# Performance work log

Measured on AMD Instinct MI355X. Metric: run time of the kernel, lower is better.

## Reference

```python
import jax, jax.numpy as jnp
import numpy as np
import math

B, W, N = 48, 100, 1000
EMB, H, QKV, LOCAL = 128, 8, 16, 100
L = LOCAL + 1  # depot + local_size neighbors


def pos_enc(length):
    # sinusoidal positional encoding, emb_dim even so no pad needed
    nts = EMB // 2
    inv = jnp.exp(jnp.arange(nts, dtype=jnp.float32) * (-math.log(10000.0) / max(nts - 1, 1)))
    pos = jnp.arange(length, dtype=jnp.float32)
    st = pos[:, None] * inv[None, :]
    return jnp.concatenate([jnp.sin(st), jnp.cos(st)], axis=1)  # [length, EMB]


def setup_inputs() -> dict:
    key = jax.random.key(0)
    ks = jax.random.split(key, 11)
    return {
        "theta": jax.random.uniform(ks[0], (B, W, N), dtype=jnp.float32),
        "dist": jax.random.uniform(ks[1], (B, W, N), dtype=jnp.float32),
        "xy": jax.random.uniform(ks[2], (B, W, N, 2), dtype=jnp.float32),
        "norm_demand": jax.random.uniform(ks[3], (B, W, N), dtype=jnp.float32),
        "ninf_mask": jnp.zeros((B, W, N), jnp.float32),
        "init_w": jax.random.normal(ks[4], (3, EMB), dtype=jnp.float32) * 0.1,
        "init_b": jnp.zeros((EMB,), jnp.float32),
        "cur_token": jax.random.uniform(ks[5], (EMB,), minval=-1.0, maxval=1.0, dtype=jnp.float32),
        "Wq": jax.random.normal(ks[6], (EMB, H * QKV), dtype=jnp.float32) * 0.05,
        "Wk": jax.random.normal(ks[7], (EMB, H * QKV), dtype=jnp.float32) * 0.05,
        "Wv": jax.random.normal(ks[8], (EMB, H * QKV), dtype=jnp.float32) * 0.05,
        "Wc_w": jax.random.normal(ks[9], (H * QKV, EMB), dtype=jnp.float32) * 0.05,
        "Wc_b": jnp.zeros((EMB,), jnp.float32),
    }


def reference(theta, dist, xy, norm_demand, ninf_mask, init_w, init_b, cur_token, Wq, Wk, Wv, Wc_w, Wc_b):
    # depot always masked: dist -= mask => depot distance -> +inf
    mask = ninf_mask.at[:, :, 0].set(-jnp.inf)
    dist_eff = dist - mask  # [B,W,N]

    # k smallest distances among non-depot nodes (topk largest=False)
    neg_vals, idx0 = jax.lax.top_k(-dist_eff[:, :, 1:], LOCAL)
    dvals = -neg_vals
    dvals = jnp.where(jnp.isinf(dvals), 0.0, dvals)
    norm_on = (jnp.max(dvals, axis=-1) != 0.0)[..., None]          # [B,W,1]
    norm_fac = jnp.max(dvals, axis=-1, keepdims=True) + 1e-6       # [B,W,1]

    depot = jnp.zeros((B, W, 1), idx0.dtype)
    idx = jnp.concatenate([depot, idx0 + 1], axis=-1)              # [B,W,L]

    g = lambda a: jnp.take_along_axis(a, idx, axis=-1)
    sd = g(dist_eff)
    sdem = g(norm_demand)
    sm = g(ninf_mask)
    sx = g(xy[..., 0])
    sy = g(xy[..., 1])

    # zero out inf entries (the masked depot slot)
    infm = jnp.isinf(sd)
    sdem = jnp.where(infm, 0.0, sdem)
    sx = jnp.where(infm, 0.0, sx)
    sy = jnp.where(infm, 0.0, sy)

    # per-(b,w) coordinate normalization by max local distance
    sx = jnp.where(norm_on, sx / norm_fac, sx)
    sy = jnp.where(norm_on, sy / norm_fac, sy)

    # euclidean + demand => 3 input features
    sorted_input = jnp.stack([sx, sy, sdem], axis=-1)              # [B,W,L,3]
    init_k = sorted_input @ init_w + init_b + pos_enc(L)[None, None]  # [B,W,L,EMB]

    # cur_token is identical for every (b,w) -> shared query per head
    q = (cur_token @ Wq).reshape(H, QKV)
    k = (init_k @ Wk).reshape(B, W, L, H, QKV)
    v = (init_k @ Wv).reshape(B, W, L, H, QKV)

    score = jnp.einsum('hd,bwlhd->bwhl', q, k) / float(np.sqrt(QKV)) + sm[:, :, None, :]
    attn = jax.nn.softmax(score, axis=-1)
    out = jnp.einsum('bwhl,bwlhd->bwhd', attn, v).reshape(B, W, H * QKV)

    mh = out @ Wc_w + Wc_b                                         # [B,W,EMB]
    score2 = jnp.einsum('bwe,bwle->bwl', mh, init_k) / float(np.sqrt(EMB))

    bi = jnp.arange(B)[:, None, None]
    wi = jnp.arange(W)[None, :, None]
    return jnp.zeros((B, W, N), score2.dtype).at[bi, wi, idx].set(score2)
```

## Files before the change

### kernel.cpp

```cpp
#include <hip/hip_runtime.h>
#include <math.h>

#define Bb   48
#define Ww   100
#define Nn   1000
#define EMB  128
#define Hh   8
#define LL   101
#define LOCALK 100
#define TPB  128
#define PPB  2

typedef float f4v __attribute__((ext_vector_type(4)));

#define WS_A    0
#define WS_PE   1024
#define WS_AC   13952
#define WS_WVI  13984
#define WS_PEA  14496
#define WS_PVT  15304
#define WS_PET  28232

#define AR_SIZE 7840
#define AR_SEL  5088
#define AR_PERM 5492
#define AR_SMK  5592
#define AR_F3   5996
#define AR_MHF  7208
#define AR_COEF 7720
#define AR_CM   7816

#define WSYNC() do { __builtin_amdgcn_wave_barrier(); asm volatile("" ::: "memory"); } while (0)

__device__ __forceinline__ unsigned f2key(float x) {
    unsigned u = __float_as_uint(x);
    return (u & 0x80000000u) ? ~u : (u | 0x80000000u);
}
__device__ __forceinline__ float key2f(unsigned k) {
    unsigned u = (k & 0x80000000u) ? (k & 0x7fffffffu) : ~k;
    return __uint_as_float(u);
}

__global__ void setup1(const float* __restrict__ cur, const float* __restrict__ Wq,
                       const float* __restrict__ Wk, const float* __restrict__ iw,
                       const float* __restrict__ ib, const float* __restrict__ Wv,
                       float* __restrict__ ws) {
    const int t = threadIdx.x, b = blockIdx.x;
    if (b == 0) {
        __shared__ float qs[EMB];
        __shared__ float as_[Hh * EMB];
        if (t < EMB) {
            float acc = 0.f;
            for (int e = 0; e < EMB; ++e) acc += cur[e] * Wq[e * EMB + t];
            qs[t] = acc;
        }
        __syncthreads();
        for (int i = t; i < Hh * EMB; i += 256) {
            int h = i >> 7, e = i & 127;
            float acc = 0.f;
            for (int d = 0; d < 16; ++d) acc += Wk[e * EMB + h * 16 + d] * qs[h * 16 + d];
            acc *= 0.25f;
            as_[i] = acc; ws[WS_A + i] = acc;
        }
        __syncthreads();
        if (t < 32) {
            int i = t >> 3, h = t & 7;
            const float* src = (i == 0) ? iw : (i == 1) ? iw + EMB : (i == 2) ? iw + 2 * EMB : ib;
            float acc = 0.f;
            for (int e = 0; e < EMB; ++e) acc += src[e] * as_[h * EMB + e];
            ws[WS_AC + t] = acc;
        }
    } else {
        int base = (b - 1) * 256 + t;
        const float kneg = -0.14619587891040738f;
        if (base < LL * EMB) {
            int l = base >> 7, c = base & 127, ic = c & 63;
            float inv = expf((float)ic * kneg);
            float v = (float)l * inv;
            ws[WS_PE + base] = (c < 64) ? sinf(v) : cosf(v);
        } else if (base < LL * EMB + 512) {
            int j = base - LL * EMB;
            int iv = j >> 7, hd = j & 127;
            const float* src = (iv == 0) ? iw : (iv == 1) ? iw + EMB : (iv == 2) ? iw + 2 * EMB : ib;
            float acc = 0.f;
            for (int e = 0; e < EMB; ++e) acc += src[e] * Wv[e * EMB + hd];
            ws[WS_WVI + j] = acc;
        }
    }
}

__global__ void setup2(const float* __restrict__ Wv, float* __restrict__ ws) {
    int idx = blockIdx.x * 256 + threadIdx.x;
    if (idx < LL * EMB) {
        int l = idx >> 7, hd = idx & 127;
        const float* pr = ws + WS_PE + l * EMB;
        float acc = 0.f;
        for (int e = 0; e < EMB; ++e) acc += pr[e] * Wv[e * EMB + hd];
        ws[WS_PVT + idx] = acc;
    } else if (idx < LL * EMB + 128 * 128) {
        int j = idx - LL * EMB;
        int e = j >> 7, l = j & 127;
        ws[WS_PET + j] = (l < LL) ? ws[WS_PE + l * EMB + e] : 0.f;
    } else if (idx < LL * EMB + 128 * 128 + Hh * LL) {
        int j = idx - (LL * EMB + 128 * 128);
        int h = j / LL, l = j - h * LL;
        const float* pr = ws + WS_PE + l * EMB;
        const float* ar = ws + WS_A + h * EMB;
        float acc = 0.f;
        for (int e = 0; e < EMB; ++e) acc += pr[e] * ar[e];
        ws[WS_PEA + j] = acc;
    }
}

__global__ __launch_bounds__(TPB, 4) void main_kernel(
    const float* __restrict__ dist,
    const float* __restrict__ xy,
    const float* __restrict__ ndem,
    const float* __restrict__ ninf,
    const float* __restrict__ iw,
    const float* __restrict__ ib,
    const float* __restrict__ Wcw,
    const float* __restrict__ Wcb,
    const float* __restrict__ ws,
    float* __restrict__ out) {

    __shared__ __align__(16) char smem[PPB][AR_SIZE];
    __shared__ __align__(16) float sPEA[Hh * LL + 32];

    const int tid  = threadIdx.x;
    const int w    = tid >> 6;
    const int lane = tid & 63;
    const int bid  = blockIdx.x;
    const int bw   = ((bid & 7) * 300 + (bid >> 3)) * PPB + w;

    for (int i = tid; i < Hh * LL + 32; i += TPB)
        sPEA[i] = (i < Hh * LL) ? ws[WS_PEA + i] : ws[WS_AC + (i - Hh * LL)];
    __syncthreads();
    const float* sAC = sPEA + Hh * LL;

    char* A = smem[w];
    int*                hist4 = (int*)A;
    float*              attnf = (float*)A;
    float*              uhf   = (float*)(A + 3232);
    float*              row   = (float*)A;
    unsigned long long* list  = (unsigned long long*)(A + 4288);
    int*                sel   = (int*)(A + AR_SEL);
    unsigned char*      perm  = (unsigned char*)(A + AR_PERM);
    float*              smk   = (float*)(A + AR_SMK);
    float*              feat3 = (float*)(A + AR_F3);
    float*              mhf   = (float*)(A + AR_MHF);
    float*              coef  = (float*)(A + AR_COEF);
    float*              coefM = (float*)(A + AR_CM);

    const float* distRow = dist + (size_t)bw * Nn;
    const float* maskRow = ninf + (size_t)bw * Nn;
    const float* xyRow   = xy   + (size_t)bw * Nn * 2;
    const float* demRow  = ndem + (size_t)bw * Nn;

    float dvf[16], mkf[16];
    {
        float4 dv[4], mv[4];
        #pragma unroll
        for (int c = 0; c < 4; ++c) {
            int n0 = c * 256 + lane * 4;
            if (n0 < Nn) {
                dv[c] = *(const float4*)(distRow + n0);
                mv[c] = *(const float4*)(maskRow + n0);
            } else {
                dv[c] = make_float4(0.f, 0.f, 0.f, 0.f);
                mv[c] = make_float4(0.f, 0.f, 0.f, 0.f);
            }
        }
        #pragma unroll
        for (int k = 0; k < 5; ++k) {
            int idx = lane + 64 * k;
            if (idx < 260) ((int4*)hist4)[idx] = make_int4(0, 0, 0, 0);
        }
        #pragma unroll
        for (int c = 0; c < 4; ++c) {
            dvf[4*c+0] = dv[c].x; dvf[4*c+1] = dv[c].y; dvf[4*c+2] = dv[c].z; dvf[4*c+3] = dv[c].w;
            mkf[4*c+0] = mv[c].x; mkf[4*c+1] = mv[c].y; mkf[4*c+2] = mv[c].z; mkf[4*c+3] = mv[c].w;
        }
    }
    unsigned long long rk[16];
    #pragma unroll
    for (int r = 0; r < 16; ++r) {
        int n = (r >> 2) * 256 + lane * 4 + (r & 3);
        unsigned long long kv = ~0ull;
        if (n >= 1 && n < Nn) {
            float de = dvf[r] - mkf[r];
            kv = ((unsigned long long)f2key(de) << 32) | (unsigned)n;
        }
        rk[r] = kv;
    }
    WSYNC();

    unsigned long long prefix = 0;
    int shift = 56;
    int remRank = 99;
    const unsigned long long ltm = (1ull << lane) - 1ull;
    const int g0 = (lane >> 4) * 260;
    for (int round = 0; round < 8; ++round) {
        shift = 56 - 8 * round;
        #pragma unroll
        for (int r = 0; r < 16; ++r) {
            unsigned long long kv = rk[r];
            bool in = (kv != ~0ull) &&
                      (round == 0 || (kv >> (shift + 8)) == (prefix >> (shift + 8)));
            if (in) atomicAdd(&hist4[g0 + (int)((kv >> shift) & 0xffull)], 1);
        }
        WSYNC();
        int4 h0 = *(int4*)&hist4[0 * 260 + 4 * lane];
        int4 h1 = *(int4*)&hist4[1 * 260 + 4 * lane];
        int4 h2 = *(int4*)&hist4[2 * 260 + 4 * lane];
        int4 h3 = *(int4*)&hist4[3 * 260 + 4 * lane];
        int4 z = make_int4(0, 0, 0, 0);
        *(int4*)&hist4[0 * 260 + 4 * lane] = z;
        *(int4*)&hist4[1 * 260 + 4 * lane] = z;
        *(int4*)&hist4[2 * 260 + 4 * lane] = z;
        *(int4*)&hist4[3 * 260 + 4 * lane] = z;
        int cx = h0.x + h1.x + h2.x + h3.x;
        int cy = h0.y + h1.y + h2.y + h3.y;
        int cz = h0.z + h1.z + h2.z + h3.z;
        int cw = h0.w + h1.w + h2.w + h3.w;
        int s = cx + cy + cz + cw;
        int incl = s;
        #pragma unroll
        for (int o = 1; o < 64; o <<= 1) { int t = __shfl_up(incl, o, 64); if (lane >= o) incl += t; }
        int e0 = incl - s;
        int e1 = e0 + cx, e2 = e1 + cy, e3 = e2 + cz;
        int bc = -1, ec = 0, cc = 0;
        if (cx > 0 && remRank >= e0 && remRank < e1)      { bc = 4*lane+0; ec = e0; cc = cx; }
        if (cy > 0 && remRank >= e1 && remRank < e2)      { bc = 4*lane+1; ec = e1; cc = cy; }
        if (cz > 0 && remRank >= e2 && remRank < e3)      { bc = 4*lane+2; ec = e2; cc = cz; }
        if (cw > 0 && remRank >= e3 && remRank < e3 + cw) { bc = 4*lane+3; ec = e3; cc = cw; }
        unsigned long long fm = __ballot(bc >= 0);
        int srcl = __ffsll((unsigned long long)fm) - 1;
        bc = __shfl(bc, srcl, 64); ec = __shfl(ec, srcl, 64); cc = __shfl(cc, srcl, 64);
        prefix |= ((unsigned long long)(unsigned)bc) << shift;
        remRank -= ec;
        if (cc == 1) break;
    }
    unsigned long long pk = 0; bool pf = false;
    #pragma unroll
    for (int r = 0; r < 16; ++r)
        if ((rk[r] >> shift) == (prefix >> shift)) { pk = rk[r]; pf = true; }
    {
        unsigned long long fm = __ballot(pf);
        int srcl = __ffsll((unsigned long long)fm) - 1;
        pk = __shfl(pk, srcl, 64);
    }
    const unsigned long long pivot = pk;

    int cnt_run = 0;
    #pragma unroll
    for (int r = 0; r < 16; ++r) {
        bool p = rk[r] <= pivot;
        unsigned long long m = __ballot(p);
        if (p) list[cnt_run + (int)__popcll(m & ltm)] = rk[r];
        cnt_run += (int)__popcll(m);
    }
    WSYNC();

    float xs[16], ys[16], dd[16];
    {
        #pragma unroll
        for (int c = 0; c < 4; ++c) {
            int n0 = c * 256 + lane * 4;
            float4 a0, a1, d0;
            if (n0 < Nn) {
                a0 = *(const float4*)(xyRow + 2 * n0);
                a1 = *(const float4*)(xyRow + 2 * n0 + 4);
                d0 = *(const float4*)(demRow + n0);
            } else {
                a0 = a1 = d0 = make_float4(0.f, 0.f, 0.f, 0.f);
            }
            xs[4*c+0] = a0.x; ys[4*c+0] = a0.y;
            xs[4*c+1] = a0.z; ys[4*c+1] = a0.w;
            xs[4*c+2] = a1.x; ys[4*c+2] = a1.y;
            xs[4*c+3] = a1.z; ys[4*c+3] = a1.w;
            dd[4*c+0] = d0.x; dd[4*c+1] = d0.y; dd[4*c+2] = d0.z; dd[4*c+3] = d0.w;
        }
    }

    {
        unsigned long long kv0 = list[lane];
        const bool has1 = lane < (LOCALK - 64);
        unsigned long long kv1 = has1 ? list[lane + 64] : ~0ull;
        int r0 = 0, r1 = 0;
        #pragma unroll 4
        for (int j = 0; j < LOCALK; ++j) {
            unsigned long long lv = list[j];
            r0 += (lv < kv0);
            r1 += (lv < kv1);
        }
        float v0 = key2f((unsigned)(kv0 >> 32));
        float dvm = isinf(v0) ? 0.f : v0;
        perm[lane] = (unsigned char)(r0 + 1);
        if (has1) {
            float v1 = key2f((unsigned)(kv1 >> 32));
            perm[lane + 64] = (unsigned char)(r1 + 1);
            dvm = fmaxf(dvm, isinf(v1) ? 0.f : v1);
        }
        #pragma unroll
        for (int o = 32; o > 0; o >>= 1) dvm = fmaxf(dvm, __shfl_xor(dvm, o, 64));
        const float nmax = dvm;
        const bool  norm_on = (nmax != 0.f);
        const float nfac = nmax + 1e-6f;
        WSYNC();

        int crun = 0;
        #pragma unroll
        for (int r = 0; r < 16; ++r) {
            unsigned long long kv = rk[r];
            bool p = kv <= pivot;
            unsigned long long m = __ballot(p);
            int pos = crun + (int)__popcll(m & ltm);
            crun += (int)__popcll(m);
            if (p) {
                int rnk = perm[pos];
                float val = key2f((unsigned)(kv >> 32));
                bool infm = isinf(val);
                float fx = infm ? 0.f : xs[r];
                float fy = infm ? 0.f : ys[r];
                float fd = infm ? 0.f : dd[r];
                if (norm_on) { fx /= nfac; fy /= nfac; }
                int n = (int)(kv & 0xffffffu);
                feat3[rnk] = fx; feat3[101 + rnk] = fy; feat3[202 + rnk] = fd;
                smk[rnk] = mkf[r];
                sel[rnk] = n | (infm ? 0x40000000 : 0);
            }
        }
        if (lane == 0) {
            feat3[0] = 0.f; feat3[101] = 0.f; feat3[202] = 0.f;
            smk[0] = mkf[0];
            sel[0] = 0x40000000;
        }
    }
    WSYNC();

    const int h = lane >> 3, ln8 = lane & 7;
    {
        const float A0 = sAC[h], A1 = sAC[8 + h], A2 = sAC[16 + h], Cc = sAC[24 + h];
        const float* pea = sPEA + h * LL;
        float ev[14];
        float mx = -INFINITY;
        #pragma unroll
        for (int k = 0; k < 14; ++k) {
            int l = ln8 + 8 * k;
            float sv = -INFINITY;
            if (l < LL)
                sv = feat3[l] * A0 + feat3[101 + l] * A1 + feat3[202 + l] * A2
                   + Cc + pea[l] + smk[l];
            ev[k] = sv;
            mx = fmaxf(mx, sv);
        }
        #pragma unroll
        for (int o = 1; o < 8; o <<= 1) mx = fmaxf(mx, __shfl_xor(mx, o, 64));
        float sm = 0.f;
        #pragma unroll
        for (int k = 0; k < 14; ++k) {
            int l = ln8 + 8 * k;
            float e = (l < LL) ? __expf(ev[k] - mx) : 0.f;
            ev[k] = e; sm += e;
        }
        #pragma unroll
        for (int o = 1; o < 8; o <<= 1) sm += __shfl_xor(sm, o, 64);
        const float ainv = 1.f / sm;
        float c0 = 0.f, c1 = 0.f, c2 = 0.f;
        #pragma unroll
        for (int k = 0; k < 14; ++k) {
            int l = ln8 + 8 * k;
            if (l < LL) {
                float at = ev[k] * ainv;
                attnf[h * LL + l] = at;
                c0 += at * feat3[l]; c1 += at * feat3[101 + l]; c2 += at * feat3[202 + l];
            }
        }
        #pragma unroll
        for (int o = 1; o < 8; o <<= 1) {
            c0 += __shfl_xor(c0, o, 64); c1 += __shfl_xor(c1, o, 64); c2 += __shfl_xor(c2, o, 64);
        }
        if (ln8 == 0) { coef[h * 3 + 0] = c0; coef[h * 3 + 1] = c1; coef[h * 3 + 2] = c2; }
    }
    WSYNC();

    {
        float u0 = 0.f, u1 = 0.f;
        const float* arow = attnf + h * LL;
        const float2* pvt = (const float2*)(ws + WS_PVT) + lane;
        #pragma unroll 4
        for (int l = 0; l < LL; ++l) {
            float a = arow[l];
            float2 p = pvt[(size_t)l * 64];
            u0 += a * p.x; u1 += a * p.y;
        }
        float2 w0 = *(const float2*)(ws + WS_WVI + 2 * lane);
        float2 w1 = *(const float2*)(ws + WS_WVI + 128 + 2 * lane);
        float2 w2 = *(const float2*)(ws + WS_WVI + 256 + 2 * lane);
        float2 w3 = *(const float2*)(ws + WS_WVI + 384 + 2 * lane);
        float cc0 = coef[h * 3 + 0], cc1 = coef[h * 3 + 1], cc2 = coef[h * 3 + 2];
        u0 += cc0 * w0.x + cc1 * w1.x + cc2 * w2.x + w3.x;
        u1 += cc0 * w0.y + cc1 * w1.y + cc2 * w2.y + w3.y;
        *(float2*)(uhf + 2 * lane) = make_float2(u0, u1);
    }
    WSYNC();

    {
        float2 wb = *(const float2*)(Wcb + 2 * lane);
        float m0 = wb.x, m1 = wb.y;
        const float2* wc = (const float2*)Wcw + lane;
        #pragma unroll 4
        for (int hd = 0; hd < EMB; ++hd) {
            float uu = uhf[hd];
            float2 wv = wc[(size_t)hd * 64];
            m0 += uu * wv.x; m1 += uu * wv.y;
        }
        *(float2*)(mhf + 2 * lane) = make_float2(m0, m1);
    }
    WSYNC();

    {
        int g = lane & 3;
        const float* src = (g == 0) ? iw : (g == 1) ? iw + EMB : (g == 2) ? iw + 2 * EMB : ib;
        float v = 0.f;
        #pragma unroll
        for (int j = 0; j < 8; ++j) {
            int e = (lane >> 2) + 16 * j;
            v += mhf[e] * src[e];
        }
        v += __shfl_xor(v, 4, 64); v += __shfl_xor(v, 8, 64);
        v += __shfl_xor(v, 16, 64); v += __shfl_xor(v, 32, 64);
        if (lane < 4) coefM[lane] = v;
    }
    {
        float4 z = make_float4(0.f, 0.f, 0.f, 0.f);
        ((float4*)row)[lane] = z;
        ((float4*)row)[lane + 64] = z;
        ((float4*)row)[lane + 128] = z;
        if (lane < 58) ((float4*)row)[lane + 192] = z;
    }
    WSYNC();

    {
        float s0 = 0.f, s1 = 0.f;
        const float* pet = ws + WS_PET;
        #pragma unroll 4
        for (int e = 0; e < EMB; ++e) {
            float mv = mhf[e];
            const float* pr = pet + (size_t)e * 128;
            s0 += mv * pr[lane];
            s1 += mv * pr[lane + 64];
        }
        const float scale = 0.08838834764831845f;
        {
            int t = lane;
            float base = feat3[t] * coefM[0] + feat3[101 + t] * coefM[1]
                       + feat3[202 + t] * coefM[2] + coefM[3];
            row[sel[t] & 0xffffff] = (base + s0) * scale;
        }
        if (lane + 64 < LL) {
            int t = lane + 64;
            float base = feat3[t] * coefM[0] + feat3[101 + t] * coefM[1]
                       + feat3[202 + t] * coefM[2] + coefM[3];
            row[sel[t] & 0xffffff] = (base + s1) * scale;
        }
    }
    WSYNC();

    float* outRow = out + (size_t)bw * Nn;
    #pragma unroll
    for (int c = 0; c < 4; ++c) {
        int i = lane + 64 * c;
        if (i < 250) {
            f4v v = *(const f4v*)(row + 4 * i);
            __builtin_nontemporal_store(v, (f4v*)(outRow + 4 * i));
        }
    }
}

extern "C" void kernel_launch(void* const* d_in, const int* in_sizes, int n_in,
                              void* d_out, int out_size, void* d_ws, size_t ws_size,
                              hipStream_t stream) {
    const float* dist  = (const float*)d_in[1];
    const float* xy    = (const float*)d_in[2];
    const float* ndem  = (const float*)d_in[3];
    const float* ninf  = (const float*)d_in[4];
    const float* initw = (const float*)d_in[5];
    const float* initb = (const float*)d_in[6];
    const float* cur   = (const float*)d_in[7];
    const float* Wq    = (const float*)d_in[8];
    const float* Wk    = (const float*)d_in[9];
    const float* Wv    = (const float*)d_in[10];
    const float* Wcw   = (const float*)d_in[11];
    const float* Wcb   = (const float*)d_in[12];
    float* out = (float*)d_out;
    float* ws  = (float*)d_ws;

    hipLaunchKernelGGL(setup1, dim3(56),  dim3(256), 0, stream, cur, Wq, Wk, initw, initb, Wv, ws);
    hipLaunchKernelGGL(setup2, dim3(118), dim3(256), 0, stream, Wv, ws);
    hipLaunchKernelGGL(main_kernel, dim3(Bb * Ww / PPB), dim3(TPB), 0, stream,
                       dist, xy, ndem, ninf, initw, initb, Wcw, Wcb, ws, out);
}
```

Measured before the change: 115.5 us.

## Split main kernel into top-k/attention stage and LDS-cached projection stage

```diff
diff --git a/kernel.cpp b/kernel.cpp
--- a/kernel.cpp
+++ b/kernel.cpp
@@ -13,22 +13,25 @@
 
 typedef float f4v __attribute__((ext_vector_type(4)));
 
-#define WS_A    0
-#define WS_PE   1024
-#define WS_AC   13952
-#define WS_WVI  13984
-#define WS_PEA  14496
-#define WS_PVT  15304
-#define WS_PET  28232
-
-#define AR_SIZE 7840
+#define WS_A     0
+#define WS_PE    1024
+#define WS_AC    13952
+#define WS_WVI   13984
+#define WS_PEA   14496
+#define WS_PVT   15304
+#define WS_GPT   21768
+#define WS_WCW   28424
+#define WS_CB    28936
+#define WS_CBPE  28940
+
+#define AR_SIZE 7360
+#define AR_LIST 4288
 #define AR_SEL  5088
-#define AR_PERM 5492
-#define AR_SMK  5592
-#define AR_F3   5996
-#define AR_MHF  7208
-#define AR_COEF 7720
-#define AR_CM   7816
+#define AR_PERM 5504
+#define AR_SMK  5616
+#define AR_F3   6032
+#define AR_COEF 7248
+
 
 #define WSYNC() do { __builtin_amdgcn_wave_barrier(); asm volatile("" ::: "memory"); } while (0)
 
@@ -39,6 +42,11 @@
 __device__ __forceinline__ float key2f(unsigned k) {
     unsigned u = (k & 0x80000000u) ? (k & 0x7fffffffu) : ~k;
     return __uint_as_float(u);
+}
+__device__ __forceinline__ unsigned short f2hbits(float x) {
+    union { _Float16 h; unsigned short u; } cv;
+    cv.h = (_Float16)x;
+    return cv.u;
 }
 
 __global__ void setup1(const float* __restrict__ cur, const float* __restrict__ Wq,
@@ -89,38 +97,64 @@
     }
 }
 
-__global__ void setup2(const float* __restrict__ Wv, float* __restrict__ ws) {
+__global__ void setup2(const float* __restrict__ Wv, const float* __restrict__ Wcw,
+                       const float* __restrict__ Wcb, const float* __restrict__ iw,
+                       const float* __restrict__ ib, float* __restrict__ ws) {
     int idx = blockIdx.x * 256 + threadIdx.x;
-    if (idx < LL * EMB) {
+    if (idx < 12928) {
         int l = idx >> 7, hd = idx & 127;
         const float* pr = ws + WS_PE + l * EMB;
         float acc = 0.f;
         for (int e = 0; e < EMB; ++e) acc += pr[e] * Wv[e * EMB + hd];
-        ws[WS_PVT + idx] = acc;
-    } else if (idx < LL * EMB + 128 * 128) {
-        int j = idx - LL * EMB;
-        int e = j >> 7, l = j & 127;
-        ws[WS_PET + j] = (l < LL) ? ws[WS_PE + l * EMB + e] : 0.f;
-    } else if (idx < LL * EMB + 128 * 128 + Hh * LL) {
-        int j = idx - (LL * EMB + 128 * 128);
+        ((_Float16*)(ws + WS_PVT))[idx] = (_Float16)acc;
+    } else if (idx < 12928 + 13312) {
+        int j = idx - 12928;
+        int hd = j / 104, l = j - hd * 104;
+        float acc = 0.f;
+        if (l < LL) {
+            const float* wr = Wcw + hd * EMB;
+            const float* pr = ws + WS_PE + l * EMB;
+            for (int e = 0; e < EMB; ++e) acc += wr[e] * pr[e];
+        }
+        ((_Float16*)(ws + WS_GPT))[j] = (_Float16)acc;
+    } else if (idx < 26240 + 808) {
+        int j = idx - 26240;
         int h = j / LL, l = j - h * LL;
         const float* pr = ws + WS_PE + l * EMB;
         const float* ar = ws + WS_A + h * EMB;
         float acc = 0.f;
         for (int e = 0; e < EMB; ++e) acc += pr[e] * ar[e];
         ws[WS_PEA + j] = acc;
-    }
-}
-
-__global__ __launch_bounds__(TPB, 4) void main_kernel(
+    } else if (idx < 27048 + 512) {
+        int j = idx - 27048;
+        int i = j >> 7, hd = j & 127;
+        const float* src = (i == 0) ? iw : (i == 1) ? iw + EMB : (i == 2) ? iw + 2 * EMB : ib;
+        const float* wr = Wcw + hd * EMB;
+        float acc = 0.f;
+        for (int e = 0; e < EMB; ++e) acc += wr[e] * src[e];
+        ws[WS_WCW + j] = acc;
+    } else if (idx < 27560 + 4) {
+        int i = idx - 27560;
+        const float* src = (i == 0) ? iw : (i == 1) ? iw + EMB : (i == 2) ? iw + 2 * EMB : ib;
+        float acc = 0.f;
+        for (int e = 0; e < EMB; ++e) acc += Wcb[e] * src[e];
+        ws[WS_CB + i] = acc;
+    } else if (idx < 27564 + 104) {
+        int l = idx - 27564;
+        float acc = 0.f;
+        if (l < LL) {
+            const float* pr = ws + WS_PE + l * EMB;
+            for (int e = 0; e < EMB; ++e) acc += Wcb[e] * pr[e];
+        }
+        ws[WS_CBPE + l] = acc;
+    }
+}
+
+__global__ __launch_bounds__(TPB, 5) void kernelA(
     const float* __restrict__ dist,
     const float* __restrict__ xy,
     const float* __restrict__ ndem,
     const float* __restrict__ ninf,
-    const float* __restrict__ iw,
-    const float* __restrict__ ib,
-    const float* __restrict__ Wcw,
-    const float* __restrict__ Wcb,
     const float* __restrict__ ws,
     float* __restrict__ out) {
 
@@ -140,17 +174,13 @@
 
     char* A = smem[w];
     int*                hist4 = (int*)A;
-    float*              attnf = (float*)A;
-    float*              uhf   = (float*)(A + 3232);
-    float*              row   = (float*)A;
-    unsigned long long* list  = (unsigned long long*)(A + 4288);
+    _Float16*           attnh = (_Float16*)A;
+    unsigned long long* list  = (unsigned long long*)(A + AR_LIST);
     int*                sel   = (int*)(A + AR_SEL);
     unsigned char*      perm  = (unsigned char*)(A + AR_PERM);
     float*              smk   = (float*)(A + AR_SMK);
     float*              feat3 = (float*)(A + AR_F3);
-    float*              mhf   = (float*)(A + AR_MHF);
-    float*              coef  = (float*)(A + AR_COEF);
-    float*              coefM = (float*)(A + AR_CM);
+    float*              coefA = (float*)(A + AR_COEF);
 
     const float* distRow = dist + (size_t)bw * Nn;
     const float* maskRow = ninf + (size_t)bw * Nn;
@@ -328,13 +358,14 @@
                 int n = (int)(kv & 0xffffffu);
                 feat3[rnk] = fx; feat3[101 + rnk] = fy; feat3[202 + rnk] = fd;
                 smk[rnk] = mkf[r];
-                sel[rnk] = n | (infm ? 0x40000000 : 0);
+                sel[rnk] = n | (infm ? 0x4000 : 0);
             }
         }
         if (lane == 0) {
-            feat3[0] = 0.f; feat3[101] = 0.f; feat3[202] = 0.f;
+            feat3[0] = 0.f; feat3[101] = 0.f; feat3[202] = 0.f; feat3[303] = 0.f;
             smk[0] = mkf[0];
-            sel[0] = 0x40000000;
+            sel[0] = 0x4000;
+            sel[101] = 0; sel[102] = 0; sel[103] = 0;
         }
     }
     WSYNC();
@@ -343,10 +374,10 @@
     {
         const float A0 = sAC[h], A1 = sAC[8 + h], A2 = sAC[16 + h], Cc = sAC[24 + h];
         const float* pea = sPEA + h * LL;
-        float ev[14];
+        float ev[13];
         float mx = -INFINITY;
         #pragma unroll
-        for (int k = 0; k < 14; ++k) {
+        for (int k = 0; k < 13; ++k) {
             int l = ln8 + 8 * k;
             float sv = -INFINITY;
             if (l < LL)
@@ -359,7 +390,7 @@
         for (int o = 1; o < 8; o <<= 1) mx = fmaxf(mx, __shfl_xor(mx, o, 64));
         float sm = 0.f;
         #pragma unroll
-        for (int k = 0; k < 14; ++k) {
+        for (int k = 0; k < 13; ++k) {
             int l = ln8 + 8 * k;
             float e = (l < LL) ? __expf(ev[k] - mx) : 0.f;
             ev[k] = e; sm += e;
@@ -369,11 +400,11 @@
         const float ainv = 1.f / sm;
         float c0 = 0.f, c1 = 0.f, c2 = 0.f;
         #pragma unroll
-        for (int k = 0; k < 14; ++k) {
+        for (int k = 0; k < 13; ++k) {
             int l = ln8 + 8 * k;
+            float at = ev[k] * ainv;
+            attnh[h * 104 + l] = (_Float16)at;
             if (l < LL) {
-                float at = ev[k] * ainv;
-                attnf[h * LL + l] = at;
                 c0 += at * feat3[l]; c1 += at * feat3[101 + l]; c2 += at * feat3[202 + l];
             }
         }
@@ -381,101 +412,140 @@
         for (int o = 1; o < 8; o <<= 1) {
             c0 += __shfl_xor(c0, o, 64); c1 += __shfl_xor(c1, o, 64); c2 += __shfl_xor(c2, o, 64);
         }
-        if (ln8 == 0) { coef[h * 3 + 0] = c0; coef[h * 3 + 1] = c1; coef[h * 3 + 2] = c2; }
+        if (ln8 == 0) { coefA[h * 3 + 0] = c0; coefA[h * 3 + 1] = c1; coefA[h * 3 + 2] = c2; }
     }
     WSYNC();
 
     {
-        float u0 = 0.f, u1 = 0.f;
-        const float* arow = attnf + h * LL;
-        const float2* pvt = (const float2*)(ws + WS_PVT) + lane;
-        #pragma unroll 4
-        for (int l = 0; l < LL; ++l) {
-            float a = arow[l];
-            float2 p = pvt[(size_t)l * 64];
-            u0 += a * p.x; u1 += a * p.y;
-        }
-        float2 w0 = *(const float2*)(ws + WS_WVI + 2 * lane);
-        float2 w1 = *(const float2*)(ws + WS_WVI + 128 + 2 * lane);
-        float2 w2 = *(const float2*)(ws + WS_WVI + 256 + 2 * lane);
-        float2 w3 = *(const float2*)(ws + WS_WVI + 384 + 2 * lane);
-        float cc0 = coef[h * 3 + 0], cc1 = coef[h * 3 + 1], cc2 = coef[h * 3 + 2];
-        u0 += cc0 * w0.x + cc1 * w1.x + cc2 * w2.x + w3.x;
-        u1 += cc0 * w0.y + cc1 * w1.y + cc2 * w2.y + w3.y;
-        *(float2*)(uhf + 2 * lane) = make_float2(u0, u1);
-    }
-    WSYNC();
-
-    {
-        float2 wb = *(const float2*)(Wcb + 2 * lane);
-        float m0 = wb.x, m1 = wb.y;
-        const float2* wc = (const float2*)Wcw + lane;
-        #pragma unroll 4
-        for (int hd = 0; hd < EMB; ++hd) {
-            float uu = uhf[hd];
-            float2 wv = wc[(size_t)hd * 64];
-            m0 += uu * wv.x; m1 += uu * wv.y;
-        }
-        *(float2*)(mhf + 2 * lane) = make_float2(m0, m1);
-    }
-    WSYNC();
-
-    {
-        int g = lane & 3;
-        const float* src = (g == 0) ? iw : (g == 1) ? iw + EMB : (g == 2) ? iw + 2 * EMB : ib;
-        float v = 0.f;
-        #pragma unroll
-        for (int j = 0; j < 8; ++j) {
-            int e = (lane >> 2) + 16 * j;
-            v += mhf[e] * src[e];
-        }
-        v += __shfl_xor(v, 4, 64); v += __shfl_xor(v, 8, 64);
-        v += __shfl_xor(v, 16, 64); v += __shfl_xor(v, 32, 64);
-        if (lane < 4) coefM[lane] = v;
-    }
-    {
-        float4 z = make_float4(0.f, 0.f, 0.f, 0.f);
-        ((float4*)row)[lane] = z;
-        ((float4*)row)[lane + 64] = z;
-        ((float4*)row)[lane + 128] = z;
-        if (lane < 58) ((float4*)row)[lane + 192] = z;
-    }
-    WSYNC();
-
-    {
-        float s0 = 0.f, s1 = 0.f;
-        const float* pet = ws + WS_PET;
-        #pragma unroll 4
-        for (int e = 0; e < EMB; ++e) {
-            float mv = mhf[e];
-            const float* pr = pet + (size_t)e * 128;
-            s0 += mv * pr[lane];
-            s1 += mv * pr[lane + 64];
-        }
-        const float scale = 0.08838834764831845f;
-        {
-            int t = lane;
-            float base = feat3[t] * coefM[0] + feat3[101 + t] * coefM[1]
-                       + feat3[202 + t] * coefM[2] + coefM[3];
-            row[sel[t] & 0xffffff] = (base + s0) * scale;
-        }
-        if (lane + 64 < LL) {
-            int t = lane + 64;
-            float base = feat3[t] * coefM[0] + feat3[101 + t] * coefM[1]
-                       + feat3[202 + t] * coefM[2] + coefM[3];
-            row[sel[t] & 0xffffff] = (base + s1) * scale;
-        }
-    }
-    WSYNC();
-
-    float* outRow = out + (size_t)bw * Nn;
-    #pragma unroll
-    for (int c = 0; c < 4; ++c) {
-        int i = lane + 64 * c;
-        if (i < 250) {
-            f4v v = *(const f4v*)(row + 4 * i);
-            __builtin_nontemporal_store(v, (f4v*)(outRow + 4 * i));
-        }
+        float* gRow = out + (size_t)bw * Nn;
+        ((int4*)gRow)[lane] = ((const int4*)attnh)[lane];
+        if (lane < 40) ((int4*)gRow)[lane + 64] = ((const int4*)attnh)[lane + 64];
+        if (lane < 38) {
+            int c = lane;
+            int wd[4];
+            #pragma unroll
+            for (int k2 = 0; k2 < 4; ++k2) {
+                unsigned lo = f2hbits(feat3[8 * c + 2 * k2]);
+                unsigned hi = f2hbits(feat3[8 * c + 2 * k2 + 1]);
+                wd[k2] = (int)(lo | (hi << 16));
+            }
+            ((int4*)(gRow + 416))[c] = make_int4(wd[0], wd[1], wd[2], wd[3]);
+        }
+        if (lane < 13) {
+            int c = lane;
+            int wd[4];
+            #pragma unroll
+            for (int k2 = 0; k2 < 4; ++k2) {
+                unsigned lo = (unsigned)sel[8 * c + 2 * k2] & 0xffffu;
+                unsigned hi = (unsigned)sel[8 * c + 2 * k2 + 1] & 0xffffu;
+                wd[k2] = (int)(lo | (hi << 16));
+            }
+            ((int4*)(gRow + 568))[c] = make_int4(wd[0], wd[1], wd[2], wd[3]);
+        }
+        if (lane < 6) ((int4*)(gRow + 620))[lane] = ((const int4*)coefA)[lane];
+    }
+}
+
+#define BG 8
+__global__ __launch_bounds__(256, 2) void kernelB(
+    const float* __restrict__ ws,
+    float* __restrict__ out) {
+
+    __shared__ __align__(16) _Float16 PVL[LL * 132];
+    __shared__ __align__(16) _Float16 GPTL[EMB * 132];
+    __shared__ __align__(16) float wcc[620];
+    __shared__ __align__(16) _Float16 attnL[832];
+    __shared__ __align__(16) _Float16 f3h[304];
+    __shared__ __align__(16) unsigned short selL[104];
+    __shared__ __align__(16) float coefL[24];
+    __shared__ __align__(16) float uf[EMB];
+    __shared__ float cM[4];
+    __shared__ __align__(16) float rowbuf[1000];
+
+    const int tid = threadIdx.x;
+    const int bid = blockIdx.x;
+    const int gb  = (bid & 7) * 75 + (bid >> 3);
+    const int p0  = gb * BG;
+
+    for (int c = tid; c < 3232; c += 256) {
+        int hi = c * 4;
+        int l = hi >> 7, col = hi & 127;
+        *(int2*)(PVL + l * 132 + col) = ((const int2*)(ws + WS_PVT))[c];
+    }
+    for (int c = tid; c < 3328; c += 256) {
+        int hi = c * 4;
+        int hd = hi / 104, col = hi - hd * 104;
+        *(int2*)(GPTL + hd * 132 + col) = ((const int2*)(ws + WS_GPT))[c];
+    }
+    for (int c = tid; c < 155; c += 256)
+        ((int4*)wcc)[c] = ((const int4*)(ws + WS_WCW))[c];
+    __syncthreads();
+
+    for (int pp = 0; pp < BG; ++pp) {
+        const int p = p0 + pp;
+        float* gRow = out + (size_t)p * Nn;
+
+        for (int c = tid; c < 161; c += 256) {
+            int4 v = ((const int4*)gRow)[c];
+            if (c < 104)       ((int4*)attnL)[c] = v;
+            else if (c < 142)  ((int4*)f3h)[c - 104] = v;
+            else if (c < 155)  ((int4*)selL)[c - 142] = v;
+            else               ((int4*)coefL)[c - 155] = v;
+        }
+        __syncthreads();
+
+        if (tid < 128) {
+            int t = tid, hh = t >> 4;
+            const _Float16* arow = attnL + hh * 104;
+            float acc = 0.f;
+            #pragma unroll 4
+            for (int l = 0; l < LL; ++l)
+                acc += (float)arow[l] * (float)PVL[l * 132 + t];
+            acc += coefL[hh * 3 + 0] * ws[WS_WVI + t]
+                 + coefL[hh * 3 + 1] * ws[WS_WVI + 128 + t]
+                 + coefL[hh * 3 + 2] * ws[WS_WVI + 256 + t]
+                 + ws[WS_WVI + 384 + t];
+            uf[t] = acc;
+        } else {
+            int z = tid - 128;
+            f4v zero = {0.f, 0.f, 0.f, 0.f};
+            #pragma unroll
+            for (int k = 0; k < 2; ++k) {
+                int i = z + 128 * k;
+                if (i < 250) *(f4v*)(rowbuf + 4 * i) = zero;
+            }
+        }
+        __syncthreads();
+
+        if (tid < 64) {
+            #pragma unroll
+            for (int i = 0; i < 4; ++i) {
+                float v = uf[tid] * wcc[i * 128 + tid] + uf[tid + 64] * wcc[i * 128 + tid + 64];
+                #pragma unroll
+                for (int o = 32; o > 0; o >>= 1) v += __shfl_xor(v, o, 64);
+                if (tid == 0) cM[i] = wcc[512 + i] + v;
+            }
+        }
+        __syncthreads();
+
+        if (tid < LL) {
+            int t = tid;
+            float acc = 0.f;
+            #pragma unroll 4
+            for (int hd = 0; hd < EMB; ++hd)
+                acc += uf[hd] * (float)GPTL[hd * 132 + t];
+            float base = (float)f3h[t] * cM[0] + (float)f3h[101 + t] * cM[1]
+                       + (float)f3h[202 + t] * cM[2] + cM[3] + wcc[516 + t];
+            int n = (int)selL[t] & 0xFFF;
+            rowbuf[n] = (base + acc) * 0.08838834764831845f;
+        }
+        __syncthreads();
+
+        for (int c = tid; c < 250; c += 256) {
+            f4v v = *(const f4v*)(rowbuf + 4 * c);
+            __builtin_nontemporal_store(v, (f4v*)(gRow + 4 * c));
+        }
+        __syncthreads();
     }
 }
 
@@ -498,7 +568,8 @@
     float* ws  = (float*)d_ws;
 
     hipLaunchKernelGGL(setup1, dim3(56),  dim3(256), 0, stream, cur, Wq, Wk, initw, initb, Wv, ws);
-    hipLaunchKernelGGL(setup2, dim3(118), dim3(256), 0, stream, Wv, ws);
-    hipLaunchKernelGGL(main_kernel, dim3(Bb * Ww / PPB), dim3(TPB), 0, stream,
-                       dist, xy, ndem, ninf, initw, initb, Wcw, Wcb, ws, out);
-}
+    hipLaunchKernelGGL(setup2, dim3(109), dim3(256), 0, stream, Wv, Wcw, Wcb, initw, initb, ws);
+    hipLaunchKernelGGL(kernelA, dim3(Bb * Ww / PPB), dim3(TPB), 0, stream,
+                       dist, xy, ndem, ninf, ws, out);
+    hipLaunchKernelGGL(kernelB, dim3(Bb * Ww / BG), dim3(256), 0, stream, ws, out);
+}
```

Result: slower. 194.8 us (+68.6%).

## Precompute Wc·PE table in fp16 and store attention/PV tables as half

Applied to the files above, without the earlier changes.

```diff
diff --git a/kernel.cpp b/kernel.cpp
--- a/kernel.cpp
+++ b/kernel.cpp
@@ -12,23 +12,27 @@
 #define PPB  2
 
 typedef float f4v __attribute__((ext_vector_type(4)));
-
-#define WS_A    0
-#define WS_PE   1024
-#define WS_AC   13952
-#define WS_WVI  13984
-#define WS_PEA  14496
-#define WS_PVT  15304
-#define WS_PET  28232
-
-#define AR_SIZE 7840
+typedef _Float16 half2v __attribute__((ext_vector_type(2)));
+
+#define WS_A     0
+#define WS_PE    1024
+#define WS_AC    13952
+#define WS_WVI   13984
+#define WS_PEA   14496
+#define WS_PVT   15304
+#define WS_GPT   21768
+#define WS_CBPE  29960
+
+#define AR_SIZE 8416
+#define AR_LIST 4288
 #define AR_SEL  5088
-#define AR_PERM 5492
-#define AR_SMK  5592
-#define AR_F3   5996
-#define AR_MHF  7208
-#define AR_COEF 7720
-#define AR_CM   7816
+#define AR_PERM 5504
+#define AR_SMK  5616
+#define AR_F3   6032
+#define AR_COEF 7248
+#define AR_UF   7360
+#define AR_MHF  7872
+#define AR_CM   8384
 
 #define WSYNC() do { __builtin_amdgcn_wave_barrier(); asm volatile("" ::: "memory"); } while (0)
 
@@ -89,30 +93,45 @@
     }
 }
 
-__global__ void setup2(const float* __restrict__ Wv, float* __restrict__ ws) {
+__global__ void setup2(const float* __restrict__ Wv, const float* __restrict__ Wcw,
+                       const float* __restrict__ Wcb, float* __restrict__ ws) {
     int idx = blockIdx.x * 256 + threadIdx.x;
-    if (idx < LL * EMB) {
+    if (idx < 12928) {
         int l = idx >> 7, hd = idx & 127;
         const float* pr = ws + WS_PE + l * EMB;
         float acc = 0.f;
         for (int e = 0; e < EMB; ++e) acc += pr[e] * Wv[e * EMB + hd];
-        ws[WS_PVT + idx] = acc;
-    } else if (idx < LL * EMB + 128 * 128) {
-        int j = idx - LL * EMB;
-        int e = j >> 7, l = j & 127;
-        ws[WS_PET + j] = (l < LL) ? ws[WS_PE + l * EMB + e] : 0.f;
-    } else if (idx < LL * EMB + 128 * 128 + Hh * LL) {
-        int j = idx - (LL * EMB + 128 * 128);
+        ((_Float16*)(ws + WS_PVT))[idx] = (_Float16)acc;
+    } else if (idx < 12928 + 16384) {
+        int j = idx - 12928;
+        int hd = j >> 7, l = j & 127;
+        float acc = 0.f;
+        if (l < LL) {
+            const float* wr = Wcw + hd * EMB;
+            const float* pr = ws + WS_PE + l * EMB;
+            for (int e = 0; e < EMB; ++e) acc += wr[e] * pr[e];
+        }
+        ((_Float16*)(ws + WS_GPT))[j] = (_Float16)acc;
+    } else if (idx < 29312 + 808) {
+        int j = idx - 29312;
         int h = j / LL, l = j - h * LL;
         const float* pr = ws + WS_PE + l * EMB;
         const float* ar = ws + WS_A + h * EMB;
         float acc = 0.f;
         for (int e = 0; e < EMB; ++e) acc += pr[e] * ar[e];
         ws[WS_PEA + j] = acc;
+    } else if (idx < 30120 + 104) {
+        int l = idx - 30120;
+        float acc = 0.f;
+        if (l < LL) {
+            const float* pr = ws + WS_PE + l * EMB;
+            for (int e = 0; e < EMB; ++e) acc += Wcb[e] * pr[e];
+        }
+        ws[WS_CBPE + l] = acc;
     }
 }
 
-__global__ __launch_bounds__(TPB, 4) void main_kernel(
+__global__ __launch_bounds__(TPB, 6) void main_kernel(
     const float* __restrict__ dist,
     const float* __restrict__ xy,
     const float* __restrict__ ndem,
@@ -140,17 +159,17 @@
 
     char* A = smem[w];
     int*                hist4 = (int*)A;
-    float*              attnf = (float*)A;
-    float*              uhf   = (float*)(A + 3232);
-    float*              row   = (float*)A;
-    unsigned long long* list  = (unsigned long long*)(A + 4288);
+    _Float16*           attnh = (_Float16*)A;
+    float*              rowbuf = (float*)A;
+    unsigned long long* list  = (unsigned long long*)(A + AR_LIST);
     int*                sel   = (int*)(A + AR_SEL);
     unsigned char*      perm  = (unsigned char*)(A + AR_PERM);
     float*              smk   = (float*)(A + AR_SMK);
     float*              feat3 = (float*)(A + AR_F3);
+    float*              coefA = (float*)(A + AR_COEF);
+    float*              uf    = (float*)(A + AR_UF);
     float*              mhf   = (float*)(A + AR_MHF);
-    float*              coef  = (float*)(A + AR_COEF);
-    float*              coefM = (float*)(A + AR_CM);
+    float*              cM    = (float*)(A + AR_CM);
 
     const float* distRow = dist + (size_t)bw * Nn;
     const float* maskRow = ninf + (size_t)bw * Nn;
@@ -328,13 +347,13 @@
                 int n = (int)(kv & 0xffffffu);
                 feat3[rnk] = fx; feat3[101 + rnk] = fy; feat3[202 + rnk] = fd;
                 smk[rnk] = mkf[r];
-                sel[rnk] = n | (infm ? 0x40000000 : 0);
+                sel[rnk] = n | (infm ? 0x4000 : 0);
             }
         }
         if (lane == 0) {
-            feat3[0] = 0.f; feat3[101] = 0.f; feat3[202] = 0.f;
+            feat3[0] = 0.f; feat3[101] = 0.f; feat3[202] = 0.f; feat3[303] = 0.f;
             smk[0] = mkf[0];
-            sel[0] = 0x40000000;
+            sel[0] = 0x4000;
         }
     }
     WSYNC();
@@ -343,10 +362,10 @@
     {
         const float A0 = sAC[h], A1 = sAC[8 + h], A2 = sAC[16 + h], Cc = sAC[24 + h];
         const float* pea = sPEA + h * LL;
-        float ev[14];
+        float ev[13];
         float mx = -INFINITY;
         #pragma unroll
-        for (int k = 0; k < 14; ++k) {
+        for (int k = 0; k < 13; ++k) {
             int l = ln8 + 8 * k;
             float sv = -INFINITY;
             if (l < LL)
@@ -359,7 +378,7 @@
         for (int o = 1; o < 8; o <<= 1) mx = fmaxf(mx, __shfl_xor(mx, o, 64));
         float sm = 0.f;
         #pragma unroll
-        for (int k = 0; k < 14; ++k) {
+        for (int k = 0; k < 13; ++k) {
             int l = ln8 + 8 * k;
             float e = (l < LL) ? __expf(ev[k] - mx) : 0.f;
             ev[k] = e; sm += e;
@@ -369,11 +388,11 @@
         const float ainv = 1.f / sm;
         float c0 = 0.f, c1 = 0.f, c2 = 0.f;
         #pragma unroll
-        for (int k = 0; k < 14; ++k) {
+        for (int k = 0; k < 13; ++k) {
             int l = ln8 + 8 * k;
+            float at = ev[k] * ainv;
+            attnh[h * 104 + l] = (_Float16)at;
             if (l < LL) {
-                float at = ev[k] * ainv;
-                attnf[h * LL + l] = at;
                 c0 += at * feat3[l]; c1 += at * feat3[101 + l]; c2 += at * feat3[202 + l];
             }
         }
@@ -381,39 +400,40 @@
         for (int o = 1; o < 8; o <<= 1) {
             c0 += __shfl_xor(c0, o, 64); c1 += __shfl_xor(c1, o, 64); c2 += __shfl_xor(c2, o, 64);
         }
-        if (ln8 == 0) { coef[h * 3 + 0] = c0; coef[h * 3 + 1] = c1; coef[h * 3 + 2] = c2; }
-    }
-    WSYNC();
-
-    {
+        if (ln8 == 0) { coefA[h * 3 + 0] = c0; coefA[h * 3 + 1] = c1; coefA[h * 3 + 2] = c2; }
+    }
+    WSYNC();
+
+    {
+        const _Float16* pv = (const _Float16*)(ws + WS_PVT) + 2 * lane;
+        const _Float16* arow = attnh + h * 104;
         float u0 = 0.f, u1 = 0.f;
-        const float* arow = attnf + h * LL;
-        const float2* pvt = (const float2*)(ws + WS_PVT) + lane;
         #pragma unroll 4
         for (int l = 0; l < LL; ++l) {
-            float a = arow[l];
-            float2 p = pvt[(size_t)l * 64];
-            u0 += a * p.x; u1 += a * p.y;
-        }
+            float a = (float)arow[l];
+            half2v p = *(const half2v*)(pv + (size_t)l * 128);
+            u0 += a * (float)p.x;
+            u1 += a * (float)p.y;
+        }
+        float cc0 = coefA[h * 3 + 0], cc1 = coefA[h * 3 + 1], cc2 = coefA[h * 3 + 2];
         float2 w0 = *(const float2*)(ws + WS_WVI + 2 * lane);
         float2 w1 = *(const float2*)(ws + WS_WVI + 128 + 2 * lane);
         float2 w2 = *(const float2*)(ws + WS_WVI + 256 + 2 * lane);
         float2 w3 = *(const float2*)(ws + WS_WVI + 384 + 2 * lane);
-        float cc0 = coef[h * 3 + 0], cc1 = coef[h * 3 + 1], cc2 = coef[h * 3 + 2];
         u0 += cc0 * w0.x + cc1 * w1.x + cc2 * w2.x + w3.x;
         u1 += cc0 * w0.y + cc1 * w1.y + cc2 * w2.y + w3.y;
-        *(float2*)(uhf + 2 * lane) = make_float2(u0, u1);
+        *(float2*)(uf + 2 * lane) = make_float2(u0, u1);
     }
     WSYNC();
 
     {
         float2 wb = *(const float2*)(Wcb + 2 * lane);
         float m0 = wb.x, m1 = wb.y;
-        const float2* wc = (const float2*)Wcw + lane;
+        const float* wc = Wcw + 2 * lane;
         #pragma unroll 4
         for (int hd = 0; hd < EMB; ++hd) {
-            float uu = uhf[hd];
-            float2 wv = wc[(size_t)hd * 64];
+            float uu = uf[hd];
+            float2 wv = *(const float2*)(wc + (size_t)hd * 128);
             m0 += uu * wv.x; m1 += uu * wv.y;
         }
         *(float2*)(mhf + 2 * lane) = make_float2(m0, m1);
@@ -431,39 +451,38 @@
         }
         v += __shfl_xor(v, 4, 64); v += __shfl_xor(v, 8, 64);
         v += __shfl_xor(v, 16, 64); v += __shfl_xor(v, 32, 64);
-        if (lane < 4) coefM[lane] = v;
+        if (lane < 4) cM[lane] = v;
     }
     {
         float4 z = make_float4(0.f, 0.f, 0.f, 0.f);
-        ((float4*)row)[lane] = z;
-        ((float4*)row)[lane + 64] = z;
-        ((float4*)row)[lane + 128] = z;
-        if (lane < 58) ((float4*)row)[lane + 192] = z;
-    }
-    WSYNC();
-
-    {
+        ((float4*)rowbuf)[lane] = z;
+        ((float4*)rowbuf)[lane + 64] = z;
+        ((float4*)rowbuf)[lane + 128] = z;
+        if (lane < 58) ((float4*)rowbuf)[lane + 192] = z;
+    }
+    WSYNC();
+
+    {
+        const _Float16* gp = (const _Float16*)(ws + WS_GPT);
         float s0 = 0.f, s1 = 0.f;
-        const float* pet = ws + WS_PET;
         #pragma unroll 4
-        for (int e = 0; e < EMB; ++e) {
-            float mv = mhf[e];
-            const float* pr = pet + (size_t)e * 128;
-            s0 += mv * pr[lane];
-            s1 += mv * pr[lane + 64];
+        for (int hd = 0; hd < EMB; ++hd) {
+            float uu = uf[hd];
+            s0 += uu * (float)gp[hd * 128 + lane];
+            s1 += uu * (float)gp[hd * 128 + lane + 64];
         }
         const float scale = 0.08838834764831845f;
         {
             int t = lane;
-            float base = feat3[t] * coefM[0] + feat3[101 + t] * coefM[1]
-                       + feat3[202 + t] * coefM[2] + coefM[3];
-            row[sel[t] & 0xffffff] = (base + s0) * scale;
+            float base = feat3[t] * cM[0] + feat3[101 + t] * cM[1]
+                       + feat3[202 + t] * cM[2] + cM[3] + ws[WS_CBPE + t];
+            rowbuf[sel[t] & 0xFFF] = (base + s0) * scale;
         }
         if (lane + 64 < LL) {
             int t = lane + 64;
-            float base = feat3[t] * coefM[0] + feat3[101 + t] * coefM[1]
-                       + feat3[202 + t] * coefM[2] + coefM[3];
-            row[sel[t] & 0xffffff] = (base + s1) * scale;
+            float base = feat3[t] * cM[0] + feat3[101 + t] * cM[1]
+                       + feat3[202 + t] * cM[2] + cM[3] + ws[WS_CBPE + t];
+            rowbuf[sel[t] & 0xFFF] = (base + s1) * scale;
         }
     }
     WSYNC();
@@ -473,7 +492,7 @@
     for (int c = 0; c < 4; ++c) {
         int i = lane + 64 * c;
         if (i < 250) {
-            f4v v = *(const f4v*)(row + 4 * i);
+            f4v v = *(const f4v*)(rowbuf + 4 * i);
             __builtin_nontemporal_store(v, (f4v*)(outRow + 4 * i));
         }
     }
@@ -498,7 +517,7 @@
     float* ws  = (float*)d_ws;
 
     hipLaunchKernelGGL(setup1, dim3(56),  dim3(256), 0, stream, cur, Wq, Wk, initw, initb, Wv, ws);
-    hipLaunchKernelGGL(setup2, dim3(118), dim3(256), 0, stream, Wv, ws);
+    hipLaunchKernelGGL(setup2, dim3(119), dim3(256), 0, stream, Wv, Wcw, Wcb, ws);
     hipLaunchKernelGGL(main_kernel, dim3(Bb * Ww / PPB), dim3(TPB), 0, stream,
                        dist, xy, ndem, ninf, initw, initb, Wcw, Wcb, ws, out);
 }
```

Result: no change. 114.5 us (-0.9%).
